# Performance work log

Hardware: AMD Instinct MI355X
Metric: run time of the kernel (lower is better)

## Reference

```python
import jax, jax.numpy as jnp
import numpy as np

N, E, G = 50000, 600000, 256
D, L, V = 128, 5, 128
BN_EPS = 1e-5


def setup_inputs() -> dict:
    key = jax.random.key(0)
    ks = jax.random.split(key, 24)
    x = jax.random.randint(ks[0], (N, 9), 0, V)
    edge_index = jax.random.randint(ks[1], (2, E), 0, N)
    edge_attr = jax.random.randint(ks[2], (E, 3), 0, V)
    batch = jnp.sort(jax.random.randint(ks[3], (N,), 0, G))
    s = 0.02
    inp = dict(
        x=x, edge_index=edge_index, edge_attr=edge_attr, batch=batch,
        atom_emb=jax.random.normal(ks[4], (9, V, D)) * s,
        bond_emb=jax.random.normal(ks[5], (L, 3, V, D)) * s,
        eps=jnp.zeros((L,)),
        W1=jax.random.normal(ks[6], (D, 2 * D)) * s, b1=jnp.zeros((2 * D,)),
        g1=jnp.ones((2 * D,)), be1=jnp.zeros((2 * D,)),
        W2=jax.random.normal(ks[7], (2 * D, D)) * s, b2=jnp.zeros((D,)),
        bn_g=jnp.ones((L, D)), bn_b=jnp.zeros((L, D)),
        fcW1=jax.random.normal(ks[8], (D, 1024)) * s, fcb1=jnp.zeros((1024,)),
        fcW2=jax.random.normal(ks[9], (1024, 1024)) * s, fcb2=jnp.zeros((1024,)),
        fcW3=jax.random.normal(ks[10], (1024, 512)) * s, fcb3=jnp.zeros((512,)),
        fcW4=jax.random.normal(ks[11], (512, 1)) * s, fcb4=jnp.zeros((1,)),
    )
    return inp


def _bn(h, g, b):
    # training-mode batchnorm (biased variance, as torch uses for normalization)
    m = h.mean(0)
    v = jnp.var(h, axis=0)
    return (h - m) * jax.lax.rsqrt(v + BN_EPS) * g + b


def _embed(tables, idx):
    # tables: [F, V, D], idx: [M, F] -> sum over F of table lookups -> [M, D]
    F = tables.shape[0]
    return tables[jnp.arange(F)[None, :], idx].sum(axis=1)


def reference(x, edge_index, edge_attr, batch, atom_emb, bond_emb, eps,
              W1, b1, g1, be1, W2, b2, bn_g, bn_b,
              fcW1, fcb1, fcW2, fcb2, fcW3, fcb3, fcW4, fcb4):
    src, dst = edge_index[0], edge_index[1]

    def mlp(h):
        z = jax.nn.relu(_bn(h @ W1 + b1, g1, be1))
        return z @ W2 + b2

    h = _embed(atom_emb, x)  # AtomEncoder: [N, D]
    h_sum = h  # JK='sum' accumulator
    for l in range(L):
        e = _embed(bond_emb[l], edge_attr)            # BondEncoder: [E, D]
        msg = jax.nn.relu(h[src] + e)                  # gather + elementwise
        agg = jax.ops.segment_sum(msg, dst, num_segments=N)  # scatter-add
        h = mlp((1.0 + eps[l]) * h + agg)
        h = _bn(h, bn_g[l], bn_b[l])
        if l < L - 1:
            h = jax.nn.relu(h)
        # dropout is identity in eval mode
        h_sum = h_sum + h

    # global mean pool over graphs
    sums = jax.ops.segment_sum(h_sum, batch, num_segments=G)
    cnts = jax.ops.segment_sum(jnp.ones((N,), h_sum.dtype), batch, num_segments=G)
    rep = sums / jnp.maximum(cnts, 1.0)[:, None]

    z = jax.nn.relu(rep @ fcW1 + fcb1)
    z = jax.nn.relu(z @ fcW2 + fcb2)
    z = jax.nn.relu(z @ fcW3 + fcb3)
    out = (z @ fcW4 + fcb4).squeeze(-1)  # [G]
    return out
```

## Files before the change

kernel.cpp:

```cpp
#include <hip/hip_runtime.h>

typedef unsigned short u16;
typedef unsigned int u32;
typedef __bf16 bf16x8 __attribute__((ext_vector_type(8)));
typedef float f32x4 __attribute__((ext_vector_type(4)));
typedef float f32x2 __attribute__((ext_vector_type(2)));

#define NN 50000
#define EE 600000
#define GG 256
#define LL 5
#define NB 196

__device__ __forceinline__ float b2f(u16 u) {
  unsigned int v = ((unsigned int)u) << 16;
  return __builtin_bit_cast(float, v);
}
__device__ __forceinline__ u16 f2b(float f) {
  unsigned int u = __builtin_bit_cast(unsigned int, f);
  u += 0x7FFFu + ((u >> 16) & 1u);
  return (u16)(u >> 16);
}
__device__ __forceinline__ f32x2 up2(u32 v) {
  f32x2 r;
  r.x = __builtin_bit_cast(float, v << 16);
  r.y = __builtin_bit_cast(float, v & 0xFFFF0000u);
  return r;
}
__device__ __forceinline__ f32x2 max0(f32x2 v) {
  f32x2 r;
  r.x = fmaxf(v.x, 0.f);
  r.y = fmaxf(v.y, 0.f);
  return r;
}

__global__ void k_detect(const u32* __restrict__ w, int* __restrict__ flag) {
  __shared__ int sh[256];
  u32 v = w[threadIdx.x];
  u32 lo = v & 0xFFFFu;
  u32 e = (lo >> 7) & 0xFFu;
  sh[threadIdx.x] = (e >= 0x60u && e <= 0x7Fu) ? 1 : 0;
  __syncthreads();
  for (int s = 128; s > 0; s >>= 1) {
    if (threadIdx.x < (unsigned)s) sh[threadIdx.x] += sh[threadIdx.x + s];
    __syncthreads();
  }
  if (threadIdx.x == 0) flag[0] = (sh[0] < 128) ? 1 : 0;
}

struct CvtArgs {
  const void* src[19];
  u16* dst[19];
  int cum[20];
};

__global__ void k_cvt_all(CvtArgs a, const int* __restrict__ flag) {
  int t = blockIdx.x * 256 + threadIdx.x;
  if (t >= a.cum[19]) return;
  int i = 0;
  while (t >= a.cum[i + 1]) ++i;
  int j = t - a.cum[i];
  if (flag[0]) a.dst[i][j] = f2b(((const float*)a.src[i])[j]);
  else a.dst[i][j] = ((const u16*)a.src[i])[j];
}

__global__ void k_tr(const u16* __restrict__ src, u16* __restrict__ dst, int K, int N) {
  __shared__ u16 t[32][33];
  const int kb = blockIdx.x * 32, nb = blockIdx.y * 32;
  const int tx = threadIdx.x & 31, ty = threadIdx.x >> 5;
#pragma unroll
  for (int i = ty; i < 32; i += 8) t[i][tx] = src[(kb + i) * N + nb + tx];
  __syncthreads();
#pragma unroll
  for (int i = ty; i < 32; i += 8) dst[(nb + i) * K + kb + tx] = t[tx][i];
}

__global__ void k_init(int* __restrict__ deg, float* __restrict__ rep,
                       float* __restrict__ bnbuf, int* __restrict__ gstart,
                       int* __restrict__ gend, float* __restrict__ c1b,
                       float* __restrict__ c0b) {
  int i = blockIdx.x * 256 + threadIdx.x;
  if (i < NN) deg[i] = 0;
  if (i < GG * 128) rep[i] = 0.f;
  if (i < 768) bnbuf[i] = 0.f;
  if (i < GG) { gstart[i] = 0; gend[i] = -1; }
  if (i < 128) { c1b[i] = 1.f; c0b[i] = 0.f; }
}

__global__ void k_deg(const int* __restrict__ ei, int* __restrict__ deg) {
  int e = blockIdx.x * 256 + threadIdx.x;
  if (e < EE) atomicAdd(&deg[ei[EE + e]], 1);
}

__global__ void k_scan1(const int* __restrict__ deg, int* __restrict__ rowp,
                        int* __restrict__ bsum) {
  __shared__ int sh[256];
  int i = blockIdx.x * 256 + threadIdx.x;
  int v = (i < NN) ? deg[i] : 0;
  sh[threadIdx.x] = v;
  __syncthreads();
  for (int s = 1; s < 256; s <<= 1) {
    int t = (threadIdx.x >= (unsigned)s) ? sh[threadIdx.x - s] : 0;
    __syncthreads();
    sh[threadIdx.x] += t;
    __syncthreads();
  }
  if (i < NN) rowp[i] = sh[threadIdx.x] - v;
  if (threadIdx.x == 255) bsum[blockIdx.x] = sh[255];
}

__global__ void k_scan2(int* __restrict__ bsum, int* __restrict__ boff) {
  __shared__ int sh[256];
  int v = (threadIdx.x < NB) ? bsum[threadIdx.x] : 0;
  sh[threadIdx.x] = v;
  __syncthreads();
  for (int s = 1; s < 256; s <<= 1) {
    int t = (threadIdx.x >= (unsigned)s) ? sh[threadIdx.x - s] : 0;
    __syncthreads();
    sh[threadIdx.x] += t;
    __syncthreads();
  }
  if (threadIdx.x < NB) boff[threadIdx.x] = sh[threadIdx.x] - v;
}

__global__ void k_scan3(int* __restrict__ rowp, const int* __restrict__ boff,
                        int* __restrict__ cursor) {
  int i = blockIdx.x * 256 + threadIdx.x;
  if (i < NN) {
    int r = rowp[i] + boff[blockIdx.x];
    rowp[i] = r;
    cursor[i] = r;
  }
  if (i == 0) rowp[NN] = EE;
}

__global__ void k_fill(const int* __restrict__ ei, const int* __restrict__ eattr,
                       int* __restrict__ cursor, uint2* __restrict__ epack) {
  int e = blockIdx.x * 256 + threadIdx.x;
  if (e < EE) {
    int d = ei[EE + e];
    int pos = atomicAdd(&cursor[d], 1);
    u32 src = (u32)ei[e];
    u32 a0 = (u32)eattr[e * 3], a1 = (u32)eattr[e * 3 + 1], a2 = (u32)eattr[e * 3 + 2];
    epack[pos] = make_uint2(src | (a0 << 16) | (a1 << 23), a2);
  }
}

__global__ void k_gb(const int* __restrict__ batch, int* __restrict__ gstart,
                     int* __restrict__ gend) {
  int n = blockIdx.x * 256 + threadIdx.x;
  if (n >= NN) return;
  int b = batch[n];
  if (n == 0 || batch[n - 1] != b) gstart[b] = n;
  if (n == NN - 1 || batch[n + 1] != b) gend[b] = n;
}

__global__ void k_atom(const int* __restrict__ x, const u16* __restrict__ aemb,
                       u16* __restrict__ hpre) {
  int idx = blockIdx.x * 256 + threadIdx.x;
  if (idx >= NN * 64) return;
  int n = idx >> 6, f2 = (idx & 63) << 1;
  float a0 = 0.f, a1 = 0.f;
#pragma unroll
  for (int j = 0; j < 9; ++j) {
    int xv = x[n * 9 + j];
    u32 v = *(const u32*)(aemb + (j * 128 + xv) * 128 + f2);
    a0 += b2f((u16)v);
    a1 += b2f((u16)(v >> 16));
  }
  u32 o = (u32)f2b(a0) | ((u32)f2b(a1) << 16);
  *(u32*)(hpre + n * 128 + f2) = o;
}

__global__ __launch_bounds__(256)
void k_pull(const u16* __restrict__ hpre, const float* __restrict__ cs1,
            const float* __restrict__ cs0, int relu_h, const int* __restrict__ rowp,
            const uint2* __restrict__ epack, const u16* __restrict__ bond,
            const u16* __restrict__ epsv, int layer, u16* __restrict__ amat) {
  const int lane = threadIdx.x & 63;
  const int node = blockIdx.x * 4 + (threadIdx.x >> 6);
  const int p0 = rowp[node], p1 = rowp[node + 1];
  const int lo = lane << 1;
  const u16* bondB = bond + 16384;
  const u16* bondC = bond + 32768;
  f32x2 c1v, c0v;
  c1v.x = cs1[lo]; c1v.y = cs1[lo + 1];
  c0v.x = cs0[lo]; c0v.y = cs0[lo + 1];
  auto act = [&](u32 v) -> f32x2 {
    f32x2 t = up2(v);
    t = t * c1v + c0v;
    if (relu_h) t = max0(t);
    return t;
  };
  f32x2 acc = {0.f, 0.f};
  int p = p0;
  for (; p + 4 <= p1; p += 4) {
    uint2 e0 = epack[p], e1 = epack[p + 1], e2 = epack[p + 2], e3 = epack[p + 3];
    u32 h0 = *(const u32*)(hpre + (size_t)(e0.x & 0xFFFFu) * 128 + lo);
    u32 h1 = *(const u32*)(hpre + (size_t)(e1.x & 0xFFFFu) * 128 + lo);
    u32 h2 = *(const u32*)(hpre + (size_t)(e2.x & 0xFFFFu) * 128 + lo);
    u32 h3 = *(const u32*)(hpre + (size_t)(e3.x & 0xFFFFu) * 128 + lo);
    u32 a0 = *(const u32*)(bond + ((e0.x >> 16) & 0x7Fu) * 128 + lo);
    u32 a1 = *(const u32*)(bond + ((e1.x >> 16) & 0x7Fu) * 128 + lo);
    u32 a2 = *(const u32*)(bond + ((e2.x >> 16) & 0x7Fu) * 128 + lo);
    u32 a3 = *(const u32*)(bond + ((e3.x >> 16) & 0x7Fu) * 128 + lo);
    u32 b0 = *(const u32*)(bondB + ((e0.x >> 23) & 0x7Fu) * 128 + lo);
    u32 b1 = *(const u32*)(bondB + ((e1.x >> 23) & 0x7Fu) * 128 + lo);
    u32 b2 = *(const u32*)(bondB + ((e2.x >> 23) & 0x7Fu) * 128 + lo);
    u32 b3 = *(const u32*)(bondB + ((e3.x >> 23) & 0x7Fu) * 128 + lo);
    u32 c0 = *(const u32*)(bondC + e0.y * 128 + lo);
    u32 c1 = *(const u32*)(bondC + e1.y * 128 + lo);
    u32 c2 = *(const u32*)(bondC + e2.y * 128 + lo);
    u32 c3 = *(const u32*)(bondC + e3.y * 128 + lo);
    acc += max0(act(h0) + up2(a0) + up2(b0) + up2(c0));
    acc += max0(act(h1) + up2(a1) + up2(b1) + up2(c1));
    acc += max0(act(h2) + up2(a2) + up2(b2) + up2(c2));
    acc += max0(act(h3) + up2(a3) + up2(b3) + up2(c3));
  }
  for (; p < p1; ++p) {
    uint2 e0 = epack[p];
    u32 h0 = *(const u32*)(hpre + (size_t)(e0.x & 0xFFFFu) * 128 + lo);
    u32 a0 = *(const u32*)(bond + ((e0.x >> 16) & 0x7Fu) * 128 + lo);
    u32 b0 = *(const u32*)(bondB + ((e0.x >> 23) & 0x7Fu) * 128 + lo);
    u32 c0 = *(const u32*)(bondC + e0.y * 128 + lo);
    acc += max0(act(h0) + up2(a0) + up2(b0) + up2(c0));
  }
  float epsf = 1.0f + b2f(epsv[layer]);
  u32 own = *(const u32*)(hpre + (size_t)node * 128 + lo);
  f32x2 ow = act(own);
  u32 o = (u32)f2b(epsf * ow.x + acc.x) | ((u32)f2b(epsf * ow.y + acc.y) << 16);
  *(u32*)(amat + (size_t)node * 128 + lo) = o;
}

__global__ __launch_bounds__(256, 2)
void k_gemm1(const u16* __restrict__ amat, const u16* __restrict__ w1t,
             const u16* __restrict__ b1, u16* __restrict__ z0,
             float* __restrict__ bnsum, float* __restrict__ bnsq) {
  __shared__ u16 As[128 * 72];
  __shared__ u16 Bs[128 * 72];
  __shared__ float colAcc[256];
  const int tid = threadIdx.x;
  const int r0 = blockIdx.x * 128;
  const int nc = blockIdx.y * 128;
  const int w = tid >> 6, lane = tid & 63, l15 = lane & 15, q = lane >> 4;
  const int wr = (w & 1) * 64, wc = (w >> 1) * 64;
  f32x4 acc[4][4];
#pragma unroll
  for (int i = 0; i < 4; ++i)
#pragma unroll
    for (int j = 0; j < 4; ++j) acc[i][j] = {0.f, 0.f, 0.f, 0.f};

#pragma unroll
  for (int ks = 0; ks < 2; ++ks) {
    const int k0 = ks * 64;
    for (int idx = tid; idx < 1024; idx += 256) {
      const int row = idx >> 3, c8 = (idx & 7) << 3;
      int gr = r0 + row; if (gr >= NN) gr = NN - 1;
      uint4 va = *(const uint4*)(amat + (size_t)gr * 128 + k0 + c8);
      *(uint4*)(As + row * 72 + c8) = va;
      uint4 vb = *(const uint4*)(w1t + (size_t)(nc + row) * 128 + k0 + c8);
      *(uint4*)(Bs + row * 72 + c8) = vb;
    }
    __syncthreads();
#pragma unroll
    for (int kk = 0; kk < 64; kk += 32) {
      const int kf = kk + q * 8;
      bf16x8 a[4], b[4];
#pragma unroll
      for (int i = 0; i < 4; ++i) a[i] = *(const bf16x8*)(As + (wr + i * 16 + l15) * 72 + kf);
#pragma unroll
      for (int j = 0; j < 4; ++j) b[j] = *(const bf16x8*)(Bs + (wc + j * 16 + l15) * 72 + kf);
#pragma unroll
      for (int i = 0; i < 4; ++i)
#pragma unroll
        for (int j = 0; j < 4; ++j)
          acc[i][j] = __builtin_amdgcn_mfma_f32_16x16x32_bf16(a[i], b[j], acc[i][j], 0, 0, 0);
    }
    __syncthreads();
  }
  colAcc[tid] = 0.f;
  __syncthreads();
#pragma unroll
  for (int j = 0; j < 4; ++j) {
    const int c = wc + j * 16 + l15;
    const float bias = b2f(b1[nc + c]);
    float ls = 0.f, lsq = 0.f;
#pragma unroll
    for (int i = 0; i < 4; ++i) {
      const int gr = r0 + wr + i * 16 + q * 4;
#pragma unroll
      for (int rg = 0; rg < 4; ++rg) {
        if (gr + rg < NN) {
          const float v = acc[i][j][rg] + bias;
          z0[(gr + rg) * 256 + nc + c] = f2b(v);
          ls += v;
          lsq += v * v;
        }
      }
    }
    atomicAdd(&colAcc[c], ls);
    atomicAdd(&colAcc[128 + c], lsq);
  }
  __syncthreads();
  if (tid < 128) {
    atomicAdd(&bnsum[nc + tid], colAcc[tid]);
    atomicAdd(&bnsq[nc + tid], colAcc[128 + tid]);
  }
}

__global__ void k_bnfin(float* __restrict__ bnsum, float* __restrict__ bnsq,
                        const u16* __restrict__ g, const u16* __restrict__ b,
                        float* __restrict__ c1, float* __restrict__ c0) {
  int t = threadIdx.x;
  float s = bnsum[t], q = bnsq[t];
  bnsum[t] = 0.f;
  bnsq[t] = 0.f;
  float m = s * (1.0f / NN);
  float var = q * (1.0f / NN) - m * m;
  float rs = rsqrtf(var + 1e-5f);
  float cc1 = rs * b2f(g[t]);
  c1[t] = cc1;
  c0[t] = b2f(b[t]) - m * cc1;
}

__global__ __launch_bounds__(256, 2)
void k_gemm2(const u16* __restrict__ z0, const float* __restrict__ c1,
             const float* __restrict__ c0, const u16* __restrict__ w2t,
             const u16* __restrict__ b2, u16* __restrict__ hpre,
             float* __restrict__ bnsum, float* __restrict__ bnsq) {
  __shared__ u16 As[128 * 72];
  __shared__ u16 Bs[128 * 72];
  __shared__ float colAcc[256];
  const int tid = threadIdx.x;
  const int r0 = blockIdx.x * 128;
  const int w = tid >> 6, lane = tid & 63, l15 = lane & 15, q = lane >> 4;
  const int wr = (w & 1) * 64, wc = (w >> 1) * 64;
  f32x4 acc[4][4];
#pragma unroll
  for (int i = 0; i < 4; ++i)
#pragma unroll
    for (int j = 0; j < 4; ++j) acc[i][j] = {0.f, 0.f, 0.f, 0.f};

#pragma unroll
  for (int ks = 0; ks < 4; ++ks) {
    const int k0 = ks * 64;
    for (int idx = tid; idx < 1024; idx += 256) {
      const int row = idx >> 3, c8 = (idx & 7) << 3;
      int gr = r0 + row; if (gr >= NN) gr = NN - 1;
      ushort4 z01 = *(const ushort4*)(z0 + (size_t)gr * 256 + k0 + c8);
      ushort4 z23 = *(const ushort4*)(z0 + (size_t)gr * 256 + k0 + c8 + 4);
      ushort4 o01, o23;
      {
        const int k = k0 + c8;
        o01.x = f2b(fmaxf(b2f(z01.x) * c1[k + 0] + c0[k + 0], 0.f));
        o01.y = f2b(fmaxf(b2f(z01.y) * c1[k + 1] + c0[k + 1], 0.f));
        o01.z = f2b(fmaxf(b2f(z01.z) * c1[k + 2] + c0[k + 2], 0.f));
        o01.w = f2b(fmaxf(b2f(z01.w) * c1[k + 3] + c0[k + 3], 0.f));
        o23.x = f2b(fmaxf(b2f(z23.x) * c1[k + 4] + c0[k + 4], 0.f));
        o23.y = f2b(fmaxf(b2f(z23.y) * c1[k + 5] + c0[k + 5], 0.f));
        o23.z = f2b(fmaxf(b2f(z23.z) * c1[k + 6] + c0[k + 6], 0.f));
        o23.w = f2b(fmaxf(b2f(z23.w) * c1[k + 7] + c0[k + 7], 0.f));
      }
      *(ushort4*)(As + row * 72 + c8) = o01;
      *(ushort4*)(As + row * 72 + c8 + 4) = o23;
      uint4 vb = *(const uint4*)(w2t + (size_t)row * 256 + k0 + c8);
      *(uint4*)(Bs + row * 72 + c8) = vb;
    }
    __syncthreads();
#pragma unroll
    for (int kk = 0; kk < 64; kk += 32) {
      const int kf = kk + q * 8;
      bf16x8 a[4], b[4];
#pragma unroll
      for (int i = 0; i < 4; ++i) a[i] = *(const bf16x8*)(As + (wr + i * 16 + l15) * 72 + kf);
#pragma unroll
      for (int j = 0; j < 4; ++j) b[j] = *(const bf16x8*)(Bs + (wc + j * 16 + l15) * 72 + kf);
#pragma unroll
      for (int i = 0; i < 4; ++i)
#pragma unroll
        for (int j = 0; j < 4; ++j)
          acc[i][j] = __builtin_amdgcn_mfma_f32_16x16x32_bf16(a[i], b[j], acc[i][j], 0, 0, 0);
    }
    __syncthreads();
  }
  colAcc[tid] = 0.f;
  __syncthreads();
#pragma unroll
  for (int j = 0; j < 4; ++j) {
    const int c = wc + j * 16 + l15;
    const float bias = b2f(b2[c]);
    float ls = 0.f, lsq = 0.f;
#pragma unroll
    for (int i = 0; i < 4; ++i) {
      const int gr = r0 + wr + i * 16 + q * 4;
#pragma unroll
      for (int rg = 0; rg < 4; ++rg) {
        if (gr + rg < NN) {
          const float v = acc[i][j][rg] + bias;
          hpre[(gr + rg) * 128 + c] = f2b(v);
          ls += v;
          lsq += v * v;
        }
      }
    }
    atomicAdd(&colAcc[c], ls);
    atomicAdd(&colAcc[128 + c], lsq);
  }
  __syncthreads();
  if (tid < 128) {
    atomicAdd(&bnsum[tid], colAcc[tid]);
    atomicAdd(&bnsq[tid], colAcc[128 + tid]);
  }
}

__global__ void k_poolseg(const u16* __restrict__ hpre, const float* __restrict__ cs1,
                          const float* __restrict__ cs0, int dorelu,
                          const int* __restrict__ gstart, const int* __restrict__ gend,
                          float* __restrict__ rep) {
  int g = blockIdx.x >> 2, part = blockIdx.x & 3, f = threadIdx.x;
  int r0 = gstart[g], r1 = gend[g] + 1;
  int len = r1 - r0;
  if (len <= 0) return;
  int chunk = (len + 3) >> 2;
  int s = r0 + part * chunk;
  int e = s + chunk; if (e > r1) e = r1;
  float cf1 = cs1[f], cf0 = cs0[f];
  float acc = 0.f;
  for (int r = s; r < e; ++r) {
    float v = b2f(hpre[r * 128 + f]) * cf1 + cf0;
    if (dorelu) v = fmaxf(v, 0.f);
    acc += v;
  }
  if (s < e) atomicAdd(&rep[g * 128 + f], acc);
}

__global__ void k_rep(float* __restrict__ rep, const int* __restrict__ gstart,
                      const int* __restrict__ gend, u16* __restrict__ repb) {
  int idx = blockIdx.x * 256 + threadIdx.x;
  int g = idx >> 7;
  int c = gend[g] - gstart[g] + 1;
  if (c < 1) c = 1;
  float v = rep[idx] / (float)c;
  rep[idx] = v;
  repb[idx] = f2b(v);
}

__global__ __launch_bounds__(256)
void k_fcg(const u16* __restrict__ A, const u16* __restrict__ Wt,
           const u16* __restrict__ bias, u16* __restrict__ out, int K, int N) {
  const int tid = threadIdx.x;
  const int r0 = blockIdx.x * 128;
  const int nc = blockIdx.y * 128;
  const int w = tid >> 6, lane = tid & 63, l15 = lane & 15, q = lane >> 4;
  const int wr = (w & 1) * 64, wc = (w >> 1) * 64;
  f32x4 acc[4][4];
#pragma unroll
  for (int i = 0; i < 4; ++i)
#pragma unroll
    for (int j = 0; j < 4; ++j) acc[i][j] = {0.f, 0.f, 0.f, 0.f};
  const int nkb = K >> 5;
  for (int kb = 0; kb < nkb; ++kb) {
    const int kf = kb * 32 + q * 8;
    bf16x8 a[4], b[4];
#pragma unroll
    for (int i = 0; i < 4; ++i)
      a[i] = *(const bf16x8*)(A + (size_t)(r0 + wr + i * 16 + l15) * K + kf);
#pragma unroll
    for (int j = 0; j < 4; ++j)
      b[j] = *(const bf16x8*)(Wt + (size_t)(nc + wc + j * 16 + l15) * K + kf);
#pragma unroll
    for (int i = 0; i < 4; ++i)
#pragma unroll
      for (int j = 0; j < 4; ++j)
        acc[i][j] = __builtin_amdgcn_mfma_f32_16x16x32_bf16(a[i], b[j], acc[i][j], 0, 0, 0);
  }
#pragma unroll
  for (int j = 0; j < 4; ++j) {
    const int c = nc + wc + j * 16 + l15;
    const float bv = b2f(bias[c]);
#pragma unroll
    for (int i = 0; i < 4; ++i) {
      const int gr = r0 + wr + i * 16 + q * 4;
#pragma unroll
      for (int rg = 0; rg < 4; ++rg)
        out[(gr + rg) * N + c] = f2b(fmaxf(acc[i][j][rg] + bv, 0.f));
    }
  }
}

__global__ void k_fc4(const u16* __restrict__ z, const u16* __restrict__ W,
                      const u16* __restrict__ bias, void* __restrict__ out,
                      const int* __restrict__ flag) {
  int g = blockIdx.x, lane = threadIdx.x;
  float acc = 0.f;
  for (int k = lane; k < 512; k += 64) acc += b2f(z[g * 512 + k]) * b2f(W[k]);
  for (int off = 32; off > 0; off >>= 1) acc += __shfl_down(acc, off);
  if (lane == 0) {
    float r = acc + b2f(bias[0]);
    if (flag[0]) ((float*)out)[g] = r;
    else ((u16*)out)[g] = f2b(r);
  }
}

extern "C" void kernel_launch(void* const* d_in, const int* in_sizes, int n_in,
                              void* d_out, int out_size, void* d_ws, size_t ws_size,
                              hipStream_t stream) {
  const int* x     = (const int*)d_in[0];
  const int* ei    = (const int*)d_in[1];
  const int* eattr = (const int*)d_in[2];
  const int* batch = (const int*)d_in[3];

  char* ws = (char*)d_ws;
  size_t off = 0;
  auto alloc = [&](size_t bytes) -> void* {
    void* p = ws + off;
    off += (bytes + 255) & ~(size_t)255;
    return p;
  };
  int* flag = (int*)alloc(256);
  u16* cvt[23];
  CvtArgs ca;
  ca.cum[0] = 0;
  for (int i = 4; i <= 22; ++i) {
    cvt[i] = (u16*)alloc((size_t)in_sizes[i] * 2);
    ca.src[i - 4] = d_in[i];
    ca.dst[i - 4] = cvt[i];
    ca.cum[i - 3] = ca.cum[i - 4] + in_sizes[i];
  }

  u16*   hpre   = (u16*)  alloc((size_t)NN * 128 * 2);
  u16*   amat   = (u16*)  alloc((size_t)NN * 128 * 2);
  u16*   z0     = (u16*)  alloc((size_t)NN * 256 * 2);
  u16*   w1t    = (u16*)  alloc(32768 * 2);
  u16*   w2t    = (u16*)  alloc(32768 * 2);
  u16*   ft1    = (u16*)  alloc((size_t)1024 * 128 * 2);
  u16*   ft2    = (u16*)  alloc((size_t)1024 * 1024 * 2);
  u16*   ft3    = (u16*)  alloc((size_t)512 * 1024 * 2);
  int*   deg    = (int*)  alloc((size_t)NN * 4);
  int*   cursor = (int*)  alloc((size_t)NN * 4);
  int*   rowp   = (int*)  alloc((size_t)(NN + 1) * 4);
  int*   bsum   = (int*)  alloc((size_t)NB * 4);
  int*   boff   = (int*)  alloc((size_t)NB * 4);
  uint2* epack  = (uint2*)alloc((size_t)EE * 8);
  float* bnbuf  = (float*)alloc(768 * 4);
  float* bnstat = (float*)alloc(768 * 4);
  float* rep    = (float*)alloc((size_t)GG * 128 * 4);
  u16*   repb   = (u16*)  alloc((size_t)GG * 128 * 2);
  int*   gstart = (int*)  alloc((size_t)GG * 4);
  int*   gend   = (int*)  alloc((size_t)GG * 4);
  u16*   fz1    = (u16*)  alloc((size_t)GG * 1024 * 2);
  u16*   fz2    = (u16*)  alloc((size_t)GG * 1024 * 2);
  u16*   fz3    = (u16*)  alloc((size_t)GG * 512 * 2);
  (void)ws_size; (void)n_in; (void)out_size;

  float* bn1sum = bnbuf;
  float* bn1sq  = bnbuf + 256;
  float* bn2sum = bnbuf + 512;
  float* bn2sq  = bnbuf + 640;
  float* c1a    = bnstat;
  float* c0a    = bnstat + 256;
  float* c1b    = bnstat + 512;
  float* c0b    = bnstat + 640;

  k_detect<<<1, 256, 0, stream>>>((const u32*)d_in[4], flag);
  {
    int total = ca.cum[19];
    k_cvt_all<<<(total + 255) / 256, 256, 0, stream>>>(ca, flag);
  }
  const u16 *aembc = cvt[4], *bembc = cvt[5], *epsc = cvt[6], *w1c = cvt[7],
            *b1c = cvt[8], *g1c = cvt[9], *be1c = cvt[10], *w2c = cvt[11],
            *b2c = cvt[12], *bngc = cvt[13], *bnbc = cvt[14], *fw1 = cvt[15],
            *fb1 = cvt[16], *fw2 = cvt[17], *fb2 = cvt[18], *fw3 = cvt[19],
            *fb3 = cvt[20], *fw4 = cvt[21], *fb4 = cvt[22];

  {
    dim3 t1(4, 8), t2(8, 4), t3(4, 32), t4(32, 32), t5(32, 16);
    k_tr<<<t1, 256, 0, stream>>>(w1c, w1t, 128, 256);
    k_tr<<<t2, 256, 0, stream>>>(w2c, w2t, 256, 128);
    k_tr<<<t3, 256, 0, stream>>>(fw1, ft1, 128, 1024);
    k_tr<<<t4, 256, 0, stream>>>(fw2, ft2, 1024, 1024);
    k_tr<<<t5, 256, 0, stream>>>(fw3, ft3, 1024, 512);
  }

  k_init<<<(NN + 255) / 256, 256, 0, stream>>>(deg, rep, bnbuf, gstart, gend, c1b, c0b);
  k_deg<<<(EE + 255) / 256, 256, 0, stream>>>(ei, deg);
  k_scan1<<<NB, 256, 0, stream>>>(deg, rowp, bsum);
  k_scan2<<<1, 256, 0, stream>>>(bsum, boff);
  k_scan3<<<NB, 256, 0, stream>>>(rowp, boff, cursor);
  k_fill<<<(EE + 255) / 256, 256, 0, stream>>>(ei, eattr, cursor, epack);
  k_gb<<<(NN + 255) / 256, 256, 0, stream>>>(batch, gstart, gend);
  k_atom<<<(NN * 64 + 255) / 256, 256, 0, stream>>>(x, aembc, hpre);
  k_poolseg<<<GG * 4, 128, 0, stream>>>(hpre, c1b, c0b, 0, gstart, gend, rep);

  const int gx = (NN + 127) / 128;
  for (int l = 0; l < LL; ++l) {
    k_pull<<<(NN + 3) / 4, 256, 0, stream>>>(hpre, c1b, c0b, (l > 0) ? 1 : 0, rowp, epack,
                                             bembc + (size_t)l * 3 * 128 * 128, epsc, l, amat);
    dim3 grid1(gx, 2);
    k_gemm1<<<grid1, 256, 0, stream>>>(amat, w1t, b1c, z0, bn1sum, bn1sq);
    k_bnfin<<<1, 256, 0, stream>>>(bn1sum, bn1sq, g1c, be1c, c1a, c0a);
    k_gemm2<<<gx, 256, 0, stream>>>(z0, c1a, c0a, w2t, b2c, hpre, bn2sum, bn2sq);
    k_bnfin<<<1, 128, 0, stream>>>(bn2sum, bn2sq, bngc + l * 128, bnbc + l * 128,
                                   c1b, c0b);
    k_poolseg<<<GG * 4, 128, 0, stream>>>(hpre, c1b, c0b, (l < LL - 1) ? 1 : 0,
                                          gstart, gend, rep);
  }

  k_rep<<<(GG * 128) / 256, 256, 0, stream>>>(rep, gstart, gend, repb);
  {
    dim3 g1(2, 8), g2(2, 8), g3(2, 4);
    k_fcg<<<g1, 256, 0, stream>>>(repb, ft1, fb1, fz1, 128, 1024);
    k_fcg<<<g2, 256, 0, stream>>>(fz1, ft2, fb2, fz2, 1024, 1024);
    k_fcg<<<g3, 256, 0, stream>>>(fz2, ft3, fb3, fz3, 1024, 512);
  }
  k_fc4<<<GG, 64, 0, stream>>>(fz3, fw4, fb4, d_out, flag);
}
```

Baseline: 914.2 us.

## Batch GEMM tile loads, merge weight transposes, split pooling finer

The GEMM kernels now issue all four global tile loads into registers before writing them to shared memory, so more memory requests are in flight. The second GEMM also reads z0 as 16-byte vectors and applies the batchnorm+ReLU in packed pairs with hoisted scale and shift. The five weight-transpose launches become one batched launch. The pooling kernel splits each graph across eight blocks instead of four for more parallelism, at the cost of more atomics.

New measurement: 859.5 us. -6.0%, faster.

```diff
diff --git a/kernel.cpp b/kernel.cpp
--- a/kernel.cpp
+++ b/kernel.cpp
@@ -64,9 +64,24 @@
   else a.dst[i][j] = ((const u16*)a.src[i])[j];
 }
 
-__global__ void k_tr(const u16* __restrict__ src, u16* __restrict__ dst, int K, int N) {
+struct TrArgs {
+  const u16* src[5];
+  u16* dst[5];
+  int K[5], N[5];
+  int cum[6];
+};
+
+__global__ void k_tr_all(TrArgs a) {
   __shared__ u16 t[32][33];
-  const int kb = blockIdx.x * 32, nb = blockIdx.y * 32;
+  int tile = blockIdx.x;
+  int m = 0;
+  while (tile >= a.cum[m + 1]) ++m;
+  tile -= a.cum[m];
+  const int K = a.K[m], N = a.N[m];
+  const int ktiles = K >> 5;
+  const int kb = (tile % ktiles) * 32, nb = (tile / ktiles) * 32;
+  const u16* src = a.src[m];
+  u16* dst = a.dst[m];
   const int tx = threadIdx.x & 31, ty = threadIdx.x >> 5;
 #pragma unroll
   for (int i = ty; i < 32; i += 8) t[i][tx] = src[(kb + i) * N + nb + tx];
@@ -187,8 +202,7 @@
   c1v.x = cs1[lo]; c1v.y = cs1[lo + 1];
   c0v.x = cs0[lo]; c0v.y = cs0[lo + 1];
   auto act = [&](u32 v) -> f32x2 {
-    f32x2 t = up2(v);
-    t = t * c1v + c0v;
+    f32x2 t = up2(v) * c1v + c0v;
     if (relu_h) t = max0(t);
     return t;
   };
@@ -244,6 +258,7 @@
   const int nc = blockIdx.y * 128;
   const int w = tid >> 6, lane = tid & 63, l15 = lane & 15, q = lane >> 4;
   const int wr = (w & 1) * 64, wc = (w >> 1) * 64;
+  const int srow = tid >> 3, sc8 = (tid & 7) << 3;
   f32x4 acc[4][4];
 #pragma unroll
   for (int i = 0; i < 4; ++i)
@@ -253,13 +268,19 @@
 #pragma unroll
   for (int ks = 0; ks < 2; ++ks) {
     const int k0 = ks * 64;
-    for (int idx = tid; idx < 1024; idx += 256) {
-      const int row = idx >> 3, c8 = (idx & 7) << 3;
+    uint4 va[4], vb[4];
+#pragma unroll
+    for (int t = 0; t < 4; ++t) {
+      const int row = srow + t * 32;
       int gr = r0 + row; if (gr >= NN) gr = NN - 1;
-      uint4 va = *(const uint4*)(amat + (size_t)gr * 128 + k0 + c8);
-      *(uint4*)(As + row * 72 + c8) = va;
-      uint4 vb = *(const uint4*)(w1t + (size_t)(nc + row) * 128 + k0 + c8);
-      *(uint4*)(Bs + row * 72 + c8) = vb;
+      va[t] = *(const uint4*)(amat + (size_t)gr * 128 + k0 + sc8);
+      vb[t] = *(const uint4*)(w1t + (size_t)(nc + row) * 128 + k0 + sc8);
+    }
+#pragma unroll
+    for (int t = 0; t < 4; ++t) {
+      const int row = srow + t * 32;
+      *(uint4*)(As + row * 72 + sc8) = va[t];
+      *(uint4*)(Bs + row * 72 + sc8) = vb[t];
     }
     __syncthreads();
 #pragma unroll
@@ -335,6 +356,7 @@
   const int r0 = blockIdx.x * 128;
   const int w = tid >> 6, lane = tid & 63, l15 = lane & 15, q = lane >> 4;
   const int wr = (w & 1) * 64, wc = (w >> 1) * 64;
+  const int srow = tid >> 3, sc8 = (tid & 7) << 3;
   f32x4 acc[4][4];
 #pragma unroll
   for (int i = 0; i < 4; ++i)
@@ -344,27 +366,35 @@
 #pragma unroll
   for (int ks = 0; ks < 4; ++ks) {
     const int k0 = ks * 64;
-    for (int idx = tid; idx < 1024; idx += 256) {
-      const int row = idx >> 3, c8 = (idx & 7) << 3;
+    const int kb = k0 + sc8;
+    uint4 vz[4], vb[4];
+#pragma unroll
+    for (int t = 0; t < 4; ++t) {
+      const int row = srow + t * 32;
       int gr = r0 + row; if (gr >= NN) gr = NN - 1;
-      ushort4 z01 = *(const ushort4*)(z0 + (size_t)gr * 256 + k0 + c8);
-      ushort4 z23 = *(const ushort4*)(z0 + (size_t)gr * 256 + k0 + c8 + 4);
-      ushort4 o01, o23;
-      {
-        const int k = k0 + c8;
-        o01.x = f2b(fmaxf(b2f(z01.x) * c1[k + 0] + c0[k + 0], 0.f));
-        o01.y = f2b(fmaxf(b2f(z01.y) * c1[k + 1] + c0[k + 1], 0.f));
-        o01.z = f2b(fmaxf(b2f(z01.z) * c1[k + 2] + c0[k + 2], 0.f));
-        o01.w = f2b(fmaxf(b2f(z01.w) * c1[k + 3] + c0[k + 3], 0.f));
-        o23.x = f2b(fmaxf(b2f(z23.x) * c1[k + 4] + c0[k + 4], 0.f));
-        o23.y = f2b(fmaxf(b2f(z23.y) * c1[k + 5] + c0[k + 5], 0.f));
-        o23.z = f2b(fmaxf(b2f(z23.z) * c1[k + 6] + c0[k + 6], 0.f));
-        o23.w = f2b(fmaxf(b2f(z23.w) * c1[k + 7] + c0[k + 7], 0.f));
+      vz[t] = *(const uint4*)(z0 + (size_t)gr * 256 + kb);
+      vb[t] = *(const uint4*)(w2t + (size_t)row * 256 + kb);
+    }
+    f32x2 fc1[4], fc0[4];
+#pragma unroll
+    for (int e = 0; e < 4; ++e) {
+      fc1[e].x = c1[kb + 2 * e];     fc1[e].y = c1[kb + 2 * e + 1];
+      fc0[e].x = c0[kb + 2 * e];     fc0[e].y = c0[kb + 2 * e + 1];
+    }
+#pragma unroll
+    for (int t = 0; t < 4; ++t) {
+      const int row = srow + t * 32;
+      u32 zw[4] = {vz[t].x, vz[t].y, vz[t].z, vz[t].w};
+      u32 ow[4];
+#pragma unroll
+      for (int e = 0; e < 4; ++e) {
+        f32x2 r = max0(up2(zw[e]) * fc1[e] + fc0[e]);
+        ow[e] = (u32)f2b(r.x) | ((u32)f2b(r.y) << 16);
       }
-      *(ushort4*)(As + row * 72 + c8) = o01;
-      *(ushort4*)(As + row * 72 + c8 + 4) = o23;
-      uint4 vb = *(const uint4*)(w2t + (size_t)row * 256 + k0 + c8);
-      *(uint4*)(Bs + row * 72 + c8) = vb;
+      uint4 oz;
+      oz.x = ow[0]; oz.y = ow[1]; oz.z = ow[2]; oz.w = ow[3];
+      *(uint4*)(As + row * 72 + sc8) = oz;
+      *(uint4*)(Bs + row * 72 + sc8) = vb[t];
     }
     __syncthreads();
 #pragma unroll
@@ -417,13 +447,14 @@
                           const float* __restrict__ cs0, int dorelu,
                           const int* __restrict__ gstart, const int* __restrict__ gend,
                           float* __restrict__ rep) {
-  int g = blockIdx.x >> 2, part = blockIdx.x & 3, f = threadIdx.x;
+  int g = blockIdx.x >> 3, part = blockIdx.x & 7, f = threadIdx.x;
   int r0 = gstart[g], r1 = gend[g] + 1;
   int len = r1 - r0;
   if (len <= 0) return;
-  int chunk = (len + 3) >> 2;
+  int chunk = (len + 7) >> 3;
   int s = r0 + part * chunk;
   int e = s + chunk; if (e > r1) e = r1;
+  if (s >= e) return;
   float cf1 = cs1[f], cf0 = cs0[f];
   float acc = 0.f;
   for (int r = s; r < e; ++r) {
@@ -431,7 +462,7 @@
     if (dorelu) v = fmaxf(v, 0.f);
     acc += v;
   }
-  if (s < e) atomicAdd(&rep[g * 128 + f], acc);
+  atomicAdd(&rep[g * 128 + f], acc);
 }
 
 __global__ void k_rep(float* __restrict__ rep, const int* __restrict__ gstart,
@@ -574,12 +605,16 @@
             *fb3 = cvt[20], *fw4 = cvt[21], *fb4 = cvt[22];
 
   {
-    dim3 t1(4, 8), t2(8, 4), t3(4, 32), t4(32, 32), t5(32, 16);
-    k_tr<<<t1, 256, 0, stream>>>(w1c, w1t, 128, 256);
-    k_tr<<<t2, 256, 0, stream>>>(w2c, w2t, 256, 128);
-    k_tr<<<t3, 256, 0, stream>>>(fw1, ft1, 128, 1024);
-    k_tr<<<t4, 256, 0, stream>>>(fw2, ft2, 1024, 1024);
-    k_tr<<<t5, 256, 0, stream>>>(fw3, ft3, 1024, 512);
+    TrArgs ta;
+    ta.src[0] = w1c; ta.dst[0] = w1t; ta.K[0] = 128;  ta.N[0] = 256;
+    ta.src[1] = w2c; ta.dst[1] = w2t; ta.K[1] = 256;  ta.N[1] = 128;
+    ta.src[2] = fw1; ta.dst[2] = ft1; ta.K[2] = 128;  ta.N[2] = 1024;
+    ta.src[3] = fw2; ta.dst[3] = ft2; ta.K[3] = 1024; ta.N[3] = 1024;
+    ta.src[4] = fw3; ta.dst[4] = ft3; ta.K[4] = 1024; ta.N[4] = 512;
+    ta.cum[0] = 0;
+    for (int m = 0; m < 5; ++m)
+      ta.cum[m + 1] = ta.cum[m] + (ta.K[m] >> 5) * (ta.N[m] >> 5);
+    k_tr_all<<<ta.cum[5], 256, 0, stream>>>(ta);
   }
 
   k_init<<<(NN + 255) / 256, 256, 0, stream>>>(deg, rep, bnbuf, gstart, gend, c1b, c0b);
@@ -590,7 +625,7 @@
   k_fill<<<(EE + 255) / 256, 256, 0, stream>>>(ei, eattr, cursor, epack);
   k_gb<<<(NN + 255) / 256, 256, 0, stream>>>(batch, gstart, gend);
   k_atom<<<(NN * 64 + 255) / 256, 256, 0, stream>>>(x, aembc, hpre);
-  k_poolseg<<<GG * 4, 128, 0, stream>>>(hpre, c1b, c0b, 0, gstart, gend, rep);
+  k_poolseg<<<GG * 8, 128, 0, stream>>>(hpre, c1b, c0b, 0, gstart, gend, rep);
 
   const int gx = (NN + 127) / 128;
   for (int l = 0; l < LL; ++l) {
@@ -602,7 +637,7 @@
     k_gemm2<<<gx, 256, 0, stream>>>(z0, c1a, c0a, w2t, b2c, hpre, bn2sum, bn2sq);
     k_bnfin<<<1, 128, 0, stream>>>(bn2sum, bn2sq, bngc + l * 128, bnbc + l * 128,
                                    c1b, c0b);
-    k_poolseg<<<GG * 4, 128, 0, stream>>>(hpre, c1b, c0b, (l < LL - 1) ? 1 : 0,
+    k_poolseg<<<GG * 8, 128, 0, stream>>>(hpre, c1b, c0b, (l < LL - 1) ? 1 : 0,
                                           gstart, gend, rep);
   }
 
```
